# Optimization experiments

Hardware: AMD Instinct MI355X
Metric: run time of the kernel (lower is better)

## Reference

```python
import jax, jax.numpy as jnp
import numpy as np

N = 50000      # nodes
E = 400000     # edges
IN = 128       # in_channels
HID = 64       # hidden_channels (per head)
H = 4          # heads
OUT = 10       # classes
G = 64         # graphs in batch


def setup_inputs() -> dict:
    key = jax.random.key(0)
    ks = jax.random.split(key, 32)
    s = 0.05
    inp = {
        "x": jax.random.normal(ks[0], (N, IN), dtype=jnp.float32),
        "edge_index": jax.random.randint(ks[1], (2, E), 0, N, dtype=jnp.int32),
        "batch": jnp.sort(jax.random.randint(ks[2], (N,), 0, G, dtype=jnp.int32)),
    }
    # TransformerConv layer 1 params (in=IN -> heads*HID)
    d1 = H * HID
    inp["Wq1"] = jax.random.normal(ks[3], (IN, d1)) * s
    inp["bq1"] = jnp.zeros((d1,), jnp.float32)
    inp["Wk1"] = jax.random.normal(ks[4], (IN, d1)) * s
    inp["bk1"] = jnp.zeros((d1,), jnp.float32)
    inp["Wv1"] = jax.random.normal(ks[5], (IN, d1)) * s
    inp["bv1"] = jnp.zeros((d1,), jnp.float32)
    inp["Ws1"] = jax.random.normal(ks[6], (IN, d1)) * s   # root/skip weight
    inp["bs1"] = jnp.zeros((d1,), jnp.float32)
    # TransformerConv layer 2 params (in=H*HID -> heads*HID)
    inp["Wq2"] = jax.random.normal(ks[7], (d1, d1)) * s
    inp["bq2"] = jnp.zeros((d1,), jnp.float32)
    inp["Wk2"] = jax.random.normal(ks[8], (d1, d1)) * s
    inp["bk2"] = jnp.zeros((d1,), jnp.float32)
    inp["Wv2"] = jax.random.normal(ks[9], (d1, d1)) * s
    inp["bv2"] = jnp.zeros((d1,), jnp.float32)
    inp["Ws2"] = jax.random.normal(ks[10], (d1, d1)) * s
    inp["bs2"] = jnp.zeros((d1,), jnp.float32)
    # final classifier
    inp["Wl"] = jax.random.normal(ks[11], (d1, OUT)) * s
    inp["bl"] = jnp.zeros((OUT,), jnp.float32)
    return inp


def transformer_conv(x, src, dst, Wq, bq, Wk, bk, Wv, bv, Ws, bs):
    """PyG TransformerConv (concat=True, root_weight=True, beta=None, eval mode).
    src = edge_index[0] (source j), dst = edge_index[1] (target i).
    """
    n = x.shape[0]
    q = (x @ Wq + bq).reshape(n, H, HID)
    k = (x @ Wk + bk).reshape(n, H, HID)
    v = (x @ Wv + bv).reshape(n, H, HID)
    # per-edge attention logits [E, H]
    alpha = jnp.einsum('ehc,ehc->eh', q[dst], k[src]) / np.sqrt(HID).astype(np.float32)
    # scatter-softmax over incoming edges of each target node
    amax = jax.ops.segment_max(alpha, dst, num_segments=n)           # [N, H], -inf for isolated
    ex = jnp.exp(alpha - amax[dst])                                   # [E, H]
    denom = jax.ops.segment_sum(ex, dst, num_segments=n) + 1e-16      # [N, H]
    w = ex / denom[dst]                                               # normalized alpha [E, H]
    # scatter-sum aggregation of weighted values
    out = jax.ops.segment_sum(w[:, :, None] * v[src], dst, num_segments=n)  # [N, H, HID]
    out = out.reshape(n, H * HID)
    return out + (x @ Ws + bs)  # root/skip connection


def reference(x, edge_index, batch,
              Wq1, bq1, Wk1, bk1, Wv1, bv1, Ws1, bs1,
              Wq2, bq2, Wk2, bk2, Wv2, bv2, Ws2, bs2,
              Wl, bl):
    src, dst = edge_index[0], edge_index[1]
    h = jax.nn.elu(transformer_conv(x, src, dst, Wq1, bq1, Wk1, bk1, Wv1, bv1, Ws1, bs1))
    h = jax.nn.elu(transformer_conv(h, src, dst, Wq2, bq2, Wk2, bk2, Wv2, bv2, Ws2, bs2))
    # global mean pool per graph
    sums = jax.ops.segment_sum(h, batch, num_segments=G)              # [G, H*HID]
    cnt = jax.ops.segment_sum(jnp.ones((h.shape[0],), h.dtype), batch, num_segments=G)
    pooled = sums / jnp.maximum(cnt, 1.0)[:, None]
    logits = pooled @ Wl + bl
    return jax.nn.log_softmax(logits, axis=-1)
```

## Files before the change

### kernel.cpp

```cpp
#include <hip/hip_runtime.h>
#include <math.h>

constexpr int NN   = 50000;
constexpr int NE   = 400000;
constexpr int INC  = 128;
constexpr int NH   = 4;
constexpr int D1   = 256;
constexpr int D4   = 1024;
constexpr int NOUT = 10;
constexpr int NG   = 64;
constexpr int NB_SCAN = (NN + 255) / 256;


typedef __attribute__((ext_vector_type(8))) short bf16x8;
typedef __attribute__((ext_vector_type(4))) float f32x4;
typedef __attribute__((ext_vector_type(2))) float f32x2;

__device__ __forceinline__ short f2b(float f) {
  union { float f; unsigned int i; } v; v.f = f;
  unsigned int x = v.i;
  return (short)((x + 0x7FFFu + ((x >> 16) & 1u)) >> 16);
}
__device__ __forceinline__ float b2f(short u) {
  union { unsigned int i; float f; } v; v.i = ((unsigned int)(unsigned short)u) << 16;
  return v.f;
}
__device__ __forceinline__ float4 ld4b(const short* p) {
  short4 u = *(const short4*)p;
  return make_float4(b2f(u.x), b2f(u.y), b2f(u.z), b2f(u.w));
}
__device__ __forceinline__ void unpack8(const int4 v, float* f) {
  union { unsigned int u; float x; } a;
  a.u = (unsigned int)v.x << 16;         f[0] = a.x;
  a.u = (unsigned int)v.x & 0xffff0000u; f[1] = a.x;
  a.u = (unsigned int)v.y << 16;         f[2] = a.x;
  a.u = (unsigned int)v.y & 0xffff0000u; f[3] = a.x;
  a.u = (unsigned int)v.z << 16;         f[4] = a.x;
  a.u = (unsigned int)v.z & 0xffff0000u; f[5] = a.x;
  a.u = (unsigned int)v.w << 16;         f[6] = a.x;
  a.u = (unsigned int)v.w & 0xffff0000u; f[7] = a.x;
}
__device__ __forceinline__ int pk_fp8x4(float a, float b, float c, float d) {
  int v = __builtin_amdgcn_cvt_pk_fp8_f32(a, b, 0, false);
  v = __builtin_amdgcn_cvt_pk_fp8_f32(c, d, v, true);
  return v;
}

__device__ __forceinline__ void gld_lds16(const short* g, short* l) {
  __builtin_amdgcn_global_load_lds(
      (const __attribute__((address_space(1))) unsigned int*)g,
      (__attribute__((address_space(3))) unsigned int*)l, 16, 0, 0);
}

__global__ void fill_i(int* __restrict__ p, int v, int n) {
  int i = blockIdx.x * 256 + threadIdx.x;
  if (i < n) p[i] = v;
}
__global__ void fill_f(float* __restrict__ p, float v, int n) {
  int i = blockIdx.x * 256 + threadIdx.x;
  if (i < n) p[i] = v;
}

constexpr int CVT_XB  = (NN * INC / 4 + 255) / 256;
constexpr int CVT_W1B = (4 * D1 * INC + 255) / 256;
constexpr int CVT_W2B = (4 * D1 * D1 + 255) / 256;

__device__ __forceinline__ void wt_one(const float* Wq, const float* Wk,
    const float* Wv, const float* Ws, short* Wt, int kbits, int i) {
  int K = 1 << kbits;
  int seg = i >> (kbits + 8);
  int idx = i & ((D1 << kbits) - 1);
  int n = idx >> kbits, k = idx & (K - 1);
  const float* W = (seg == 0) ? Wq : (seg == 1) ? Wk : (seg == 2) ? Wv : Ws;
  int row;
  if (seg == 0)      row = n;
  else if (seg == 3) row = 768 + n;
  else               row = 256 + (n >> 2) * 8 + ((seg == 2) ? 4 : 0) + (n & 3);
  Wt[(size_t)row * K + k] = f2b(W[(size_t)k * D1 + n]);
}

__global__ void cvt_all_k(const float* __restrict__ x, short* __restrict__ Xb,
    const float* __restrict__ Wq1, const float* __restrict__ Wk1,
    const float* __restrict__ Wv1, const float* __restrict__ Ws1,
    const float* __restrict__ Wq2, const float* __restrict__ Wk2,
    const float* __restrict__ Wv2, const float* __restrict__ Ws2,
    short* __restrict__ Wtc1, short* __restrict__ Wtc2,
    const float* __restrict__ bq1, const float* __restrict__ bk1,
    const float* __restrict__ bv1, const float* __restrict__ bs1,
    const float* __restrict__ bq2, const float* __restrict__ bk2,
    const float* __restrict__ bv2, const float* __restrict__ bs2,
    float* __restrict__ bc1, float* __restrict__ bc2) {
  const int b = blockIdx.x;
  const int t = threadIdx.x;
  if (b < CVT_XB) {
    int i = (b * 256 + t) * 4;
    if (i >= NN * INC) return;
    float4 v = *(const float4*)(x + i);
    short4 o; o.x = f2b(v.x); o.y = f2b(v.y); o.z = f2b(v.z); o.w = f2b(v.w);
    *(short4*)(Xb + i) = o;
  } else if (b < CVT_XB + CVT_W1B) {
    int i = (b - CVT_XB) * 256 + t;
    if (i < 4 * D1 * INC) wt_one(Wq1, Wk1, Wv1, Ws1, Wtc1, 7, i);
  } else if (b < CVT_XB + CVT_W1B + CVT_W2B) {
    int i = (b - CVT_XB - CVT_W1B) * 256 + t;
    if (i < 4 * D1 * D1) wt_one(Wq2, Wk2, Wv2, Ws2, Wtc2, 8, i);
  } else {
    int i = (b - CVT_XB - CVT_W1B - CVT_W2B) * 256 + t;
    if (i >= 2 * D4) return;
    int row = i & (D4 - 1);
    const float* bq = (i < D4) ? bq1 : bq2;
    const float* bk = (i < D4) ? bk1 : bk2;
    const float* bv = (i < D4) ? bv1 : bv2;
    const float* bs = (i < D4) ? bs1 : bs2;
    float v;
    if (row < 256) v = bq[row];
    else if (row < 768) {
      int j = row - 256, grp = j >> 3, off = j & 7;
      int ch = grp * 4 + (off & 3);
      v = (off < 4) ? bk[ch] : bv[ch];
    } else v = bs[row - 768];
    ((i < D4) ? bc1 : bc2)[row] = v;
  }
}

__global__ void deg_count(const int* __restrict__ dst, int* __restrict__ deg) {
  int e = blockIdx.x * 256 + threadIdx.x;
  if (e < NE) atomicAdd(&deg[dst[e]], 1);
}
__global__ __launch_bounds__(256) void scan1(const int* __restrict__ deg,
    int* __restrict__ partial, const int* __restrict__ batch, int* __restrict__ gb) {
  if (blockIdx.x == NB_SCAN) {
    int g = threadIdx.x;
    if (g > NG) return;
    int lo = 0, hi = NN;
    while (lo < hi) {
      int mid = (lo + hi) >> 1;
      if (batch[mid] < g) lo = mid + 1; else hi = mid;
    }
    gb[g] = lo;
    return;
  }
  __shared__ int sh[256];
  int t = threadIdx.x, i = blockIdx.x * 256 + t;
  sh[t] = (i < NN) ? deg[i] : 0;
  __syncthreads();
  for (int off = 128; off > 0; off >>= 1) {
    if (t < off) sh[t] += sh[t + off];
    __syncthreads();
  }
  if (t == 0) partial[blockIdx.x] = sh[0];
}
__global__ __launch_bounds__(256) void scan3(const int* __restrict__ deg,
    const int* __restrict__ partial, int* __restrict__ rowstart,
    int* __restrict__ cursor) {
  __shared__ int sh[256];
  __shared__ int base_s;
  const int t = threadIdx.x;
  int pv = (t < NB_SCAN) ? partial[t] : 0;
  sh[t] = pv;
  __syncthreads();
  for (int off = 1; off < 256; off <<= 1) {
    int o = (t >= off) ? sh[t - off] : 0;
    __syncthreads();
    sh[t] += o;
    __syncthreads();
  }
  if (t == 0) base_s = (blockIdx.x == 0) ? 0 : sh[blockIdx.x - 1];
  __syncthreads();
  const int base = base_s;
  __syncthreads();
  int i = blockIdx.x * 256 + t;
  int v = (i < NN) ? deg[i] : 0;
  sh[t] = v;
  __syncthreads();
  for (int off = 1; off < 256; off <<= 1) {
    int o = (t >= off) ? sh[t - off] : 0;
    __syncthreads();
    sh[t] += o;
    __syncthreads();
  }
  int excl = sh[t] - v + base;
  if (i <= NN) rowstart[i] = excl;
  if (i < NN)  cursor[i]   = excl;
}
__global__ void scatter_k(const int* __restrict__ src, const int* __restrict__ dst,
    int* __restrict__ cursor, int* __restrict__ esrc) {
  int e = blockIdx.x * 256 + threadIdx.x;
  if (e >= NE) return;
  int d = dst[e];
  int pos = atomicAdd(&cursor[d], 1);
  esrc[pos] = src[e];
}

constexpr int CLDS = 136;

__global__ __launch_bounds__(256) void gemm_mfma(
    const short* __restrict__ Xb, const short* __restrict__ Wt,
    const float* __restrict__ bias, short* __restrict__ QS,
    unsigned char* __restrict__ KV8, int M, int K) {
  __shared__ short smem[128 * CLDS];
  short* As0 = smem;
  short* As1 = smem + 4096;
  short* Bs0 = smem + 8192;
  short* Bs1 = smem + 12288;
  const int bx = blockIdx.x;
  const int by = blockIdx.y;
  const int m_tile = (bx & 7) + (by << 3);
  const int n_tile = bx >> 3;
  const int m0 = m_tile * 128;
  if (m0 >= M) return;
  const int n0 = n_tile * 128;

  const int t    = threadIdx.x;
  const int lane = t & 63;
  const int wv   = t >> 6;
  const int wm   = (wv >> 1) * 64;
  const int wn   = (wv & 1) * 64;
  const int quad = lane >> 4;
  const int l16  = lane & 15;
  const int lrow = lane >> 2;
  const int lseg = lane & 3;

  f32x4 acc[4][4] = {};
  for (int k0 = 0; k0 < K; k0 += 64) {
#pragma unroll
    for (int j = 0; j < 2; ++j) {
      const int rb = wv * 32 + j * 16;
      int gm = m0 + rb + lrow;
      gm = gm < M ? gm : M - 1;
      const size_t ga = (size_t)gm * K + k0 + lseg * 8;
      gld_lds16(Xb + ga,      &As0[rb * 32]);
      gld_lds16(Xb + ga + 32, &As1[rb * 32]);
      const size_t gw = (size_t)(n0 + rb + lrow) * K + k0 + lseg * 8;
      gld_lds16(Wt + gw,      &Bs0[rb * 32]);
      gld_lds16(Wt + gw + 32, &Bs1[rb * 32]);
    }
    __syncthreads();
    {
      bf16x8 a[4], b[4];
#pragma unroll
      for (int mi = 0; mi < 4; mi++)
        a[mi] = *(const bf16x8*)(&As0[(wm + mi * 16 + l16) * 32 + quad * 8]);
#pragma unroll
      for (int nj = 0; nj < 4; nj++)
        b[nj] = *(const bf16x8*)(&Bs0[(wn + nj * 16 + l16) * 32 + quad * 8]);
#pragma unroll
      for (int mi = 0; mi < 4; mi++)
#pragma unroll
        for (int nj = 0; nj < 4; nj++)
          acc[mi][nj] = __builtin_amdgcn_mfma_f32_16x16x32_bf16(a[mi], b[nj], acc[mi][nj], 0, 0, 0);
#pragma unroll
      for (int mi = 0; mi < 4; mi++)
        a[mi] = *(const bf16x8*)(&As1[(wm + mi * 16 + l16) * 32 + quad * 8]);
#pragma unroll
      for (int nj = 0; nj < 4; nj++)
        b[nj] = *(const bf16x8*)(&Bs1[(wn + nj * 16 + l16) * 32 + quad * 8]);
#pragma unroll
      for (int mi = 0; mi < 4; mi++)
#pragma unroll
        for (int nj = 0; nj < 4; nj++)
          acc[mi][nj] = __builtin_amdgcn_mfma_f32_16x16x32_bf16(a[mi], b[nj], acc[mi][nj], 0, 0, 0);
    }
    __syncthreads();
  }
  float bcol[4];
#pragma unroll
  for (int nj = 0; nj < 4; nj++) bcol[nj] = bias[n0 + wn + nj * 16 + l16];
#pragma unroll
  for (int mi = 0; mi < 4; mi++)
#pragma unroll
    for (int r = 0; r < 4; r++) {
      const int row = wm + mi * 16 + quad * 4 + r;
#pragma unroll
      for (int nj = 0; nj < 4; nj++)
        smem[row * CLDS + wn + nj * 16 + l16] = f2b(acc[mi][nj][r] + bcol[nj]);
    }
  __syncthreads();
  const bool isKV = (n_tile >= 2) && (n_tile <= 5);
  const int qs_base = (n_tile < 2) ? n0 : (n0 - 512);
  const int kv_base = n0 - 256;
#pragma unroll
  for (int it = 0; it < 8; ++it) {
    const int chunk = it * 256 + t;
    const int row = chunk >> 4;
    const int cc  = (chunk & 15) * 8;
    const int gm  = m0 + row;
    if (gm >= M) continue;
    const int4 s4 = *(const int4*)(&smem[row * CLDS + cc]);
    if (isKV) {
      float f[8];
      unpack8(s4, f);
      int lo = pk_fp8x4(f[0], f[1], f[2], f[3]);
      int hi = pk_fp8x4(f[4], f[5], f[6], f[7]);
      *(int2*)(KV8 + (size_t)gm * 512 + kv_base + cc) = make_int2(lo, hi);
    } else {
      *(int4*)(QS + (size_t)gm * 512 + qs_base + cc) = s4;
    }
  }
}

template <typename TOUT>
__device__ __forceinline__ void st1(TOUT* p, float v);
template <> __device__ __forceinline__ void st1<float>(float* p, float v) { *p = v; }
template <> __device__ __forceinline__ void st1<short>(short* p, float v) { *p = f2b(v); }

__device__ __forceinline__ void dec_kv(const int2 x, float* k, float* v) {
  f32x2 a = __builtin_amdgcn_cvt_pk_f32_fp8(x.x, false);
  f32x2 b = __builtin_amdgcn_cvt_pk_f32_fp8(x.x, true);
  f32x2 c = __builtin_amdgcn_cvt_pk_f32_fp8(x.y, false);
  f32x2 d = __builtin_amdgcn_cvt_pk_f32_fp8(x.y, true);
  k[0] = a.x; k[1] = a.y; k[2] = b.x; k[3] = b.y;
  v[0] = c.x; v[1] = c.y; v[2] = d.x; v[3] = d.y;
}

template <typename TOUT>
__global__ __launch_bounds__(256) void node_attn(
    const int* __restrict__ rowstart, const int* __restrict__ esrc,
    const short* __restrict__ QS, const unsigned char* __restrict__ KV8,
    TOUT* __restrict__ out) {
  const int nid = blockIdx.x * 4 + (threadIdx.x >> 6);
  if (nid >= NN) return;
  const int t  = threadIdx.x & 63;
  const int c0 = t * 4;
  const int r0 = rowstart[nid], r1 = rowstart[nid + 1];
  const float4 q = ld4b(QS + (size_t)nid * 512 + c0);
  const unsigned char* kvb = KV8 + t * 8;
  float m = -INFINITY, denom = 0.f;
  float4 acc = make_float4(0.f, 0.f, 0.f, 0.f);
  int r = r0;
  for (; r + 3 < r1; r += 4) {
    const int2 x0 = *(const int2*)(kvb + (size_t)esrc[r + 0] * 512);
    const int2 x1 = *(const int2*)(kvb + (size_t)esrc[r + 1] * 512);
    const int2 x2 = *(const int2*)(kvb + (size_t)esrc[r + 2] * 512);
    const int2 x3 = *(const int2*)(kvb + (size_t)esrc[r + 3] * 512);
    float k0[4], v0[4], k1[4], v1[4], k2[4], v2[4], k3[4], v3[4];
    dec_kv(x0, k0, v0); dec_kv(x1, k1, v1);
    dec_kv(x2, k2, v2); dec_kv(x3, k3, v3);
    float d0 = q.x * k0[0] + q.y * k0[1] + q.z * k0[2] + q.w * k0[3];
    float d1 = q.x * k1[0] + q.y * k1[1] + q.z * k1[2] + q.w * k1[3];
    float d2 = q.x * k2[0] + q.y * k2[1] + q.z * k2[2] + q.w * k2[3];
    float d3 = q.x * k3[0] + q.y * k3[1] + q.z * k3[2] + q.w * k3[3];
#pragma unroll
    for (int off = 1; off <= 8; off <<= 1) {
      d0 += __shfl_xor(d0, off, 16);
      d1 += __shfl_xor(d1, off, 16);
      d2 += __shfl_xor(d2, off, 16);
      d3 += __shfl_xor(d3, off, 16);
    }
    d0 *= 0.125f; d1 *= 0.125f; d2 *= 0.125f; d3 *= 0.125f;
    const float nm = fmaxf(fmaxf(m, fmaxf(d0, d1)), fmaxf(d2, d3));
    const float sc = __expf(m - nm);
    const float e0 = __expf(d0 - nm);
    const float e1 = __expf(d1 - nm);
    const float e2 = __expf(d2 - nm);
    const float e3 = __expf(d3 - nm);
    denom = denom * sc + e0 + e1 + e2 + e3;
    acc.x = acc.x * sc + e0 * v0[0] + e1 * v1[0] + e2 * v2[0] + e3 * v3[0];
    acc.y = acc.y * sc + e0 * v0[1] + e1 * v1[1] + e2 * v2[1] + e3 * v3[1];
    acc.z = acc.z * sc + e0 * v0[2] + e1 * v1[2] + e2 * v2[2] + e3 * v3[2];
    acc.w = acc.w * sc + e0 * v0[3] + e1 * v1[3] + e2 * v2[3] + e3 * v3[3];
    m = nm;
  }
  for (; r < r1; r++) {
    const int2 x0 = *(const int2*)(kvb + (size_t)esrc[r] * 512);
    float k0[4], v0[4];
    dec_kv(x0, k0, v0);
    float d0 = q.x * k0[0] + q.y * k0[1] + q.z * k0[2] + q.w * k0[3];
#pragma unroll
    for (int off = 1; off <= 8; off <<= 1) d0 += __shfl_xor(d0, off, 16);
    d0 *= 0.125f;
    const float nm = fmaxf(m, d0);
    const float sc = __expf(m - nm);
    const float e0 = __expf(d0 - nm);
    denom = denom * sc + e0;
    acc.x = acc.x * sc + e0 * v0[0];
    acc.y = acc.y * sc + e0 * v0[1];
    acc.z = acc.z * sc + e0 * v0[2];
    acc.w = acc.w * sc + e0 * v0[3];
    m = nm;
  }
  const float inv = 1.0f / (denom + 1e-16f);
  const float4 sk = ld4b(QS + (size_t)nid * 512 + 256 + c0);
  float o0 = acc.x * inv + sk.x;
  float o1 = acc.y * inv + sk.y;
  float o2 = acc.z * inv + sk.z;
  float o3 = acc.w * inv + sk.w;
  o0 = o0 > 0.f ? o0 : expm1f(o0);
  o1 = o1 > 0.f ? o1 : expm1f(o1);
  o2 = o2 > 0.f ? o2 : expm1f(o2);
  o3 = o3 > 0.f ? o3 : expm1f(o3);
  TOUT* p = out + (size_t)nid * D1 + c0;
  st1<TOUT>(p + 0, o0); st1<TOUT>(p + 1, o1);
  st1<TOUT>(p + 2, o2); st1<TOUT>(p + 3, o3);
}

__global__ __launch_bounds__(256) void pool_k(const float* __restrict__ h,
    const int* __restrict__ batch, float* __restrict__ sums) {
  const int c = threadIdx.x;
  const int n0 = blockIdx.x * 64;
  const int n1 = min(n0 + 64, NN);
  float run = 0.f;
  int curg = -1;
  for (int n = n0; n < n1; n++) {
    int g = batch[n];
    if (g != curg) {
      if (curg >= 0) atomicAdd(&sums[(size_t)curg * D1 + c], run);
      run = 0.f; curg = g;
    }
    run += h[(size_t)n * D1 + c];
  }
  if (curg >= 0) atomicAdd(&sums[(size_t)curg * D1 + c], run);
}

__global__ __launch_bounds__(640) void head_k(const float* __restrict__ sums,
    const int* __restrict__ gb, const float* __restrict__ Wl,
    const float* __restrict__ bl, float* __restrict__ out) {
  __shared__ float logits[NG][NOUT];
  const int t = threadIdx.x;
  if (t < NG * NOUT) {
    int g = t / NOUT, o = t % NOUT;
    float inv = 1.0f / fmaxf((float)(gb[g + 1] - gb[g]), 1.0f);
    float acc = 0.f;
    for (int k = 0; k < D1; k++) acc += sums[(size_t)g * D1 + k] * Wl[k * NOUT + o];
    logits[g][o] = acc * inv + bl[o];
  }
  __syncthreads();
  if (t < NG) {
    float mx = -INFINITY;
#pragma unroll
    for (int o = 0; o < NOUT; o++) mx = fmaxf(mx, logits[t][o]);
    float s = 0.f;
#pragma unroll
    for (int o = 0; o < NOUT; o++) s += __expf(logits[t][o] - mx);
    float lse = mx + logf(s);
#pragma unroll
    for (int o = 0; o < NOUT; o++) out[t * NOUT + o] = logits[t][o] - lse;
  }
}

extern "C" void kernel_launch(void* const* d_in, const int* in_sizes, int n_in,
                              void* d_out, int out_size, void* d_ws, size_t ws_size,
                              hipStream_t stream) {
  const float* x   = (const float*)d_in[0];
  const int* ei    = (const int*)d_in[1];
  const int* batch = (const int*)d_in[2];
  const float* Wq1 = (const float*)d_in[3];  const float* bq1 = (const float*)d_in[4];
  const float* Wk1 = (const float*)d_in[5];  const float* bk1 = (const float*)d_in[6];
  const float* Wv1 = (const float*)d_in[7];  const float* bv1 = (const float*)d_in[8];
  const float* Ws1 = (const float*)d_in[9];  const float* bs1 = (const float*)d_in[10];
  const float* Wq2 = (const float*)d_in[11]; const float* bq2 = (const float*)d_in[12];
  const float* Wk2 = (const float*)d_in[13]; const float* bk2 = (const float*)d_in[14];
  const float* Wv2 = (const float*)d_in[15]; const float* bv2 = (const float*)d_in[16];
  const float* Ws2 = (const float*)d_in[17]; const float* bs2 = (const float*)d_in[18];
  const float* Wl  = (const float*)d_in[19]; const float* bl  = (const float*)d_in[20];

  const int* srcIdx = ei;
  const int* dstIdx = ei + NE;

  float* ws = (float*)d_ws;
  const size_t SZ_NODE = (size_t)NN * D1;
  float* H2f  = ws;
  float* sums = ws + SZ_NODE;
  float* bc1  = sums + (size_t)NG * D1;
  float* bc2  = bc1 + D4;
  short* Xb   = (short*)(bc2 + D4);
  short* H1b  = Xb + (size_t)NN * INC;
  short* QS   = H1b + SZ_NODE;
  short* Wtc1 = QS + (size_t)NN * 512;
  short* Wtc2 = Wtc1 + (size_t)D4 * INC;
  unsigned char* KV8 = (unsigned char*)(Wtc2 + (size_t)D4 * D1);
  int* ip      = (int*)(KV8 + (size_t)NN * 512);
  int* deg     = ip;
  int* partial = deg + NN;
  int* rowstart= partial + 256;
  int* cursor  = rowstart + NN + 1;
  int* esrc    = cursor + NN;
  int* gb      = esrc + NE;

  const int mtiles = (NN + 127) / 128;
  const dim3 gemmGrid(64, (mtiles + 7) / 8);
  const int edgeBlocks = (NE + 255) / 256;
  const int nodeBlocks = (NN + 255) / 256;
  const int aggBlocks  = (NN + 3) / 4;
  const int cvtBlocks  = CVT_XB + CVT_W1B + CVT_W2B + 8;

  cvt_all_k<<<cvtBlocks, 256, 0, stream>>>(x, Xb,
      Wq1, Wk1, Wv1, Ws1, Wq2, Wk2, Wv2, Ws2, Wtc1, Wtc2,
      bq1, bk1, bv1, bs1, bq2, bk2, bv2, bs2, bc1, bc2);

  fill_i<<<nodeBlocks, 256, 0, stream>>>(deg, 0, NN);
  deg_count<<<edgeBlocks, 256, 0, stream>>>(dstIdx, deg);
  scan1<<<NB_SCAN + 1, 256, 0, stream>>>(deg, partial, batch, gb);
  scan3<<<NB_SCAN, 256, 0, stream>>>(deg, partial, rowstart, cursor);
  scatter_k<<<edgeBlocks, 256, 0, stream>>>(srcIdx, dstIdx, cursor, esrc);

  gemm_mfma<<<gemmGrid, 256, 0, stream>>>(Xb, Wtc1, bc1, QS, KV8, NN, INC);
  node_attn<short><<<aggBlocks, 256, 0, stream>>>(rowstart, esrc, QS, KV8, H1b);

  gemm_mfma<<<gemmGrid, 256, 0, stream>>>(H1b, Wtc2, bc2, QS, KV8, NN, D1);
  node_attn<float><<<aggBlocks, 256, 0, stream>>>(rowstart, esrc, QS, KV8, H2f);

  fill_f<<<(NG * D1 + 255) / 256, 256, 0, stream>>>(sums, 0.f, NG * D1);
  pool_k<<<(NN + 63) / 64, 256, 0, stream>>>(H2f, batch, sums);
  head_k<<<1, 640, 0, stream>>>(sums, gb, Wl, bl, (float*)d_out);
}
```

Baseline: 370.1 us.

## Fuse mean pooling into layer-2 attention and fold fills into conversion kernel

Layer-2 node attention now reduces its four nodes per block in shared memory and atomically adds the result into per-graph sums. This removes the full fp32 H2 buffer and the separate pool kernel. The deg and sums zeroing moves into the conversion kernel, removing two launches, and layer-1 outputs are stored as packed short4. The trade-off is far more global atomics on a small set of per-graph addresses, which may contend.

```diff
diff --git a/kernel.cpp b/kernel.cpp
--- a/kernel.cpp
+++ b/kernel.cpp
@@ -52,18 +52,12 @@
       (__attribute__((address_space(3))) unsigned int*)l, 16, 0, 0);
 }
 
-__global__ void fill_i(int* __restrict__ p, int v, int n) {
-  int i = blockIdx.x * 256 + threadIdx.x;
-  if (i < n) p[i] = v;
-}
-__global__ void fill_f(float* __restrict__ p, float v, int n) {
-  int i = blockIdx.x * 256 + threadIdx.x;
-  if (i < n) p[i] = v;
-}
-
 constexpr int CVT_XB  = (NN * INC / 4 + 255) / 256;
 constexpr int CVT_W1B = (4 * D1 * INC + 255) / 256;
 constexpr int CVT_W2B = (4 * D1 * D1 + 255) / 256;
+constexpr int CVT_BB  = 8;
+constexpr int CVT_DB  = (NN + 255) / 256;
+constexpr int CVT_SB  = (NG * D1 + 255) / 256;
 
 __device__ __forceinline__ void wt_one(const float* Wq, const float* Wk,
     const float* Wv, const float* Ws, short* Wt, int kbits, int i) {
@@ -89,7 +83,8 @@
     const float* __restrict__ bv1, const float* __restrict__ bs1,
     const float* __restrict__ bq2, const float* __restrict__ bk2,
     const float* __restrict__ bv2, const float* __restrict__ bs2,
-    float* __restrict__ bc1, float* __restrict__ bc2) {
+    float* __restrict__ bc1, float* __restrict__ bc2,
+    int* __restrict__ deg, float* __restrict__ sums) {
   const int b = blockIdx.x;
   const int t = threadIdx.x;
   if (b < CVT_XB) {
@@ -104,7 +99,7 @@
   } else if (b < CVT_XB + CVT_W1B + CVT_W2B) {
     int i = (b - CVT_XB - CVT_W1B) * 256 + t;
     if (i < 4 * D1 * D1) wt_one(Wq2, Wk2, Wv2, Ws2, Wtc2, 8, i);
-  } else {
+  } else if (b < CVT_XB + CVT_W1B + CVT_W2B + CVT_BB) {
     int i = (b - CVT_XB - CVT_W1B - CVT_W2B) * 256 + t;
     if (i >= 2 * D4) return;
     int row = i & (D4 - 1);
@@ -120,6 +115,12 @@
       v = (off < 4) ? bk[ch] : bv[ch];
     } else v = bs[row - 768];
     ((i < D4) ? bc1 : bc2)[row] = v;
+  } else if (b < CVT_XB + CVT_W1B + CVT_W2B + CVT_BB + CVT_DB) {
+    int i = (b - CVT_XB - CVT_W1B - CVT_W2B - CVT_BB) * 256 + t;
+    if (i < NN) deg[i] = 0;
+  } else {
+    int i = (b - CVT_XB - CVT_W1B - CVT_W2B - CVT_BB - CVT_DB) * 256 + t;
+    if (i < NG * D1) sums[i] = 0.f;
   }
 }
 
@@ -299,11 +300,6 @@
   }
 }
 
-template <typename TOUT>
-__device__ __forceinline__ void st1(TOUT* p, float v);
-template <> __device__ __forceinline__ void st1<float>(float* p, float v) { *p = v; }
-template <> __device__ __forceinline__ void st1<short>(short* p, float v) { *p = f2b(v); }
-
 __device__ __forceinline__ void dec_kv(const int2 x, float* k, float* v) {
   f32x2 a = __builtin_amdgcn_cvt_pk_f32_fp8(x.x, false);
   f32x2 b = __builtin_amdgcn_cvt_pk_f32_fp8(x.x, true);
@@ -313,14 +309,9 @@
   v[0] = c.x; v[1] = c.y; v[2] = d.x; v[3] = d.y;
 }
 
-template <typename TOUT>
-__global__ __launch_bounds__(256) void node_attn(
+__device__ __forceinline__ float4 attn_body(int nid, int t,
     const int* __restrict__ rowstart, const int* __restrict__ esrc,
-    const short* __restrict__ QS, const unsigned char* __restrict__ KV8,
-    TOUT* __restrict__ out) {
-  const int nid = blockIdx.x * 4 + (threadIdx.x >> 6);
-  if (nid >= NN) return;
-  const int t  = threadIdx.x & 63;
+    const short* __restrict__ QS, const unsigned char* __restrict__ KV8) {
   const int c0 = t * 4;
   const int r0 = rowstart[nid], r1 = rowstart[nid + 1];
   const float4 q = ld4b(QS + (size_t)nid * 512 + c0);
@@ -381,35 +372,63 @@
   }
   const float inv = 1.0f / (denom + 1e-16f);
   const float4 sk = ld4b(QS + (size_t)nid * 512 + 256 + c0);
-  float o0 = acc.x * inv + sk.x;
-  float o1 = acc.y * inv + sk.y;
-  float o2 = acc.z * inv + sk.z;
-  float o3 = acc.w * inv + sk.w;
-  o0 = o0 > 0.f ? o0 : expm1f(o0);
-  o1 = o1 > 0.f ? o1 : expm1f(o1);
-  o2 = o2 > 0.f ? o2 : expm1f(o2);
-  o3 = o3 > 0.f ? o3 : expm1f(o3);
-  TOUT* p = out + (size_t)nid * D1 + c0;
-  st1<TOUT>(p + 0, o0); st1<TOUT>(p + 1, o1);
-  st1<TOUT>(p + 2, o2); st1<TOUT>(p + 3, o3);
-}
-
-__global__ __launch_bounds__(256) void pool_k(const float* __restrict__ h,
+  float4 o;
+  o.x = acc.x * inv + sk.x;
+  o.y = acc.y * inv + sk.y;
+  o.z = acc.z * inv + sk.z;
+  o.w = acc.w * inv + sk.w;
+  o.x = o.x > 0.f ? o.x : expm1f(o.x);
+  o.y = o.y > 0.f ? o.y : expm1f(o.y);
+  o.z = o.z > 0.f ? o.z : expm1f(o.z);
+  o.w = o.w > 0.f ? o.w : expm1f(o.w);
+  return o;
+}
+
+__global__ __launch_bounds__(256) void node_attn(
+    const int* __restrict__ rowstart, const int* __restrict__ esrc,
+    const short* __restrict__ QS, const unsigned char* __restrict__ KV8,
+    short* __restrict__ out) {
+  const int nid = blockIdx.x * 4 + (threadIdx.x >> 6);
+  if (nid >= NN) return;
+  const int t = threadIdx.x & 63;
+  float4 o = attn_body(nid, t, rowstart, esrc, QS, KV8);
+  short4 s; s.x = f2b(o.x); s.y = f2b(o.y); s.z = f2b(o.z); s.w = f2b(o.w);
+  *(short4*)(out + (size_t)nid * D1 + t * 4) = s;
+}
+
+__global__ __launch_bounds__(256) void node_attn_pool(
+    const int* __restrict__ rowstart, const int* __restrict__ esrc,
+    const short* __restrict__ QS, const unsigned char* __restrict__ KV8,
     const int* __restrict__ batch, float* __restrict__ sums) {
-  const int c = threadIdx.x;
-  const int n0 = blockIdx.x * 64;
-  const int n1 = min(n0 + 64, NN);
-  float run = 0.f;
-  int curg = -1;
-  for (int n = n0; n < n1; n++) {
-    int g = batch[n];
+  __shared__ float ob[4][D1];
+  __shared__ int og[4];
+  const int w = threadIdx.x >> 6;
+  const int t = threadIdx.x & 63;
+  const int nid = blockIdx.x * 4 + w;
+  float4 o = attn_body(nid, t, rowstart, esrc, QS, KV8);
+  *(float4*)(&ob[w][t * 4]) = o;
+  if (t == 0) og[w] = batch[nid];
+  __syncthreads();
+  if (w != 0) return;
+  const int c0 = t * 4;
+  float4 run = *(const float4*)(&ob[0][c0]);
+  int curg = og[0];
+#pragma unroll
+  for (int i = 1; i < 4; i++) {
+    const int g = og[i];
+    const float4 v = *(const float4*)(&ob[i][c0]);
     if (g != curg) {
-      if (curg >= 0) atomicAdd(&sums[(size_t)curg * D1 + c], run);
-      run = 0.f; curg = g;
-    }
-    run += h[(size_t)n * D1 + c];
-  }
-  if (curg >= 0) atomicAdd(&sums[(size_t)curg * D1 + c], run);
+      float* s = &sums[(size_t)curg * D1 + c0];
+      atomicAdd(s + 0, run.x); atomicAdd(s + 1, run.y);
+      atomicAdd(s + 2, run.z); atomicAdd(s + 3, run.w);
+      run = make_float4(0.f, 0.f, 0.f, 0.f);
+      curg = g;
+    }
+    run.x += v.x; run.y += v.y; run.z += v.z; run.w += v.w;
+  }
+  float* s = &sums[(size_t)curg * D1 + c0];
+  atomicAdd(s + 0, run.x); atomicAdd(s + 1, run.y);
+  atomicAdd(s + 2, run.z); atomicAdd(s + 3, run.w);
 }
 
 __global__ __launch_bounds__(640) void head_k(const float* __restrict__ sums,
@@ -458,14 +477,12 @@
   const int* dstIdx = ei + NE;
 
   float* ws = (float*)d_ws;
-  const size_t SZ_NODE = (size_t)NN * D1;
-  float* H2f  = ws;
-  float* sums = ws + SZ_NODE;
+  float* sums = ws;
   float* bc1  = sums + (size_t)NG * D1;
   float* bc2  = bc1 + D4;
   short* Xb   = (short*)(bc2 + D4);
   short* H1b  = Xb + (size_t)NN * INC;
-  short* QS   = H1b + SZ_NODE;
+  short* QS   = H1b + (size_t)NN * D1;
   short* Wtc1 = QS + (size_t)NN * 512;
   short* Wtc2 = Wtc1 + (size_t)D4 * INC;
   unsigned char* KV8 = (unsigned char*)(Wtc2 + (size_t)D4 * D1);
@@ -480,27 +497,23 @@
   const int mtiles = (NN + 127) / 128;
   const dim3 gemmGrid(64, (mtiles + 7) / 8);
   const int edgeBlocks = (NE + 255) / 256;
-  const int nodeBlocks = (NN + 255) / 256;
   const int aggBlocks  = (NN + 3) / 4;
-  const int cvtBlocks  = CVT_XB + CVT_W1B + CVT_W2B + 8;
+  const int cvtBlocks  = CVT_XB + CVT_W1B + CVT_W2B + CVT_BB + CVT_DB + CVT_SB;
 
   cvt_all_k<<<cvtBlocks, 256, 0, stream>>>(x, Xb,
       Wq1, Wk1, Wv1, Ws1, Wq2, Wk2, Wv2, Ws2, Wtc1, Wtc2,
-      bq1, bk1, bv1, bs1, bq2, bk2, bv2, bs2, bc1, bc2);
-
-  fill_i<<<nodeBlocks, 256, 0, stream>>>(deg, 0, NN);
+      bq1, bk1, bv1, bs1, bq2, bk2, bv2, bs2, bc1, bc2, deg, sums);
+
   deg_count<<<edgeBlocks, 256, 0, stream>>>(dstIdx, deg);
   scan1<<<NB_SCAN + 1, 256, 0, stream>>>(deg, partial, batch, gb);
   scan3<<<NB_SCAN, 256, 0, stream>>>(deg, partial, rowstart, cursor);
   scatter_k<<<edgeBlocks, 256, 0, stream>>>(srcIdx, dstIdx, cursor, esrc);
 
   gemm_mfma<<<gemmGrid, 256, 0, stream>>>(Xb, Wtc1, bc1, QS, KV8, NN, INC);
-  node_attn<short><<<aggBlocks, 256, 0, stream>>>(rowstart, esrc, QS, KV8, H1b);
+  node_attn<<<aggBlocks, 256, 0, stream>>>(rowstart, esrc, QS, KV8, H1b);
 
   gemm_mfma<<<gemmGrid, 256, 0, stream>>>(H1b, Wtc2, bc2, QS, KV8, NN, D1);
-  node_attn<float><<<aggBlocks, 256, 0, stream>>>(rowstart, esrc, QS, KV8, H2f);
-
-  fill_f<<<(NG * D1 + 255) / 256, 256, 0, stream>>>(sums, 0.f, NG * D1);
-  pool_k<<<(NN + 63) / 64, 256, 0, stream>>>(H2f, batch, sums);
+  node_attn_pool<<<aggBlocks, 256, 0, stream>>>(rowstart, esrc, QS, KV8, batch, sums);
+
   head_k<<<1, 640, 0, stream>>>(sums, gb, Wl, bl, (float*)d_out);
 }
```

Result: slower. 419.6 us (+13.4%).
